# Optimization experiments

Hardware: AMD Instinct MI355X
Metric: run time of the kernel (lower is better)

Reference implementation:

```python
import jax, jax.numpy as jnp
import numpy as np

TAU = 1.0
EPS = 1e-06


def setup_inputs() -> dict:
    key = jax.random.key(0)
    batch = jax.random.normal(key, (8192, 256), dtype=jnp.float32)
    return {"batch": batch}


def reference(batch):
    n = batch.shape[0]
    half = n // 2
    # reorder: interleave first half and second half -> [x0, y0, x1, y1, ...]
    idx = jnp.stack([jnp.arange(half), jnp.arange(half) + half], axis=1).reshape(-1)
    x = batch[idx]                                   # [n, d]

    sim = x @ x.T                                    # [n, n] raw dot products
    norm = jnp.linalg.norm(x, axis=1, keepdims=True) # [n, 1]
    normmat = norm @ norm.T                          # [n, n]

    # denominator: zero the diagonal BEFORE exp (diag contributes exp(0)=1, as in torch code)
    mask = 1.0 - jnp.eye(n, dtype=x.dtype)
    den = jnp.sum(jnp.exp(mask * sim / (normmat + EPS) / TAU), axis=1)  # [n]

    # numerator: for row k, positive pair is (i, i+1) with i = 2*(k//2); no eps (faithful)
    i = (jnp.arange(n) // 2) * 2
    num = sim[i, i + 1] / normmat[i, i + 1]          # [n]

    loss = jnp.sum(-jnp.log(jnp.exp(num / TAU) / den)) / n
    return loss
```

## Files before the change

kernel.cpp:

```cpp
#include <hip/hip_runtime.h>
#include <hip/hip_bf16.h>


#define N_ROWS 8192
#define HALF   4096
#define DDIM   256
#define NBLK   64

typedef unsigned int   u32;
typedef unsigned short u16;
typedef __attribute__((ext_vector_type(4))) float f32x4;
typedef __attribute__((ext_vector_type(8))) short bf16x8;

__device__ __forceinline__ u16 f2bf(float f) {
    u32 u = __builtin_bit_cast(u32, f);
    u32 r = u + 0x7FFFu + ((u >> 16) & 1u);
    return (u16)(r >> 16);
}

__global__ __launch_bounds__(256) void prep_kernel(const float* __restrict__ x,
                                                   u16* __restrict__ xn,
                                                   float* __restrict__ norms,
                                                   float* __restrict__ dots) {
    const int w = threadIdx.x >> 6, l = threadIdx.x & 63;
    if (blockIdx.x < 2048) {
        const int row = blockIdx.x * 4 + w;
        const float4 v = reinterpret_cast<const float4*>(x + (size_t)row * DDIM)[l];
        float sq = v.x * v.x + v.y * v.y + v.z * v.z + v.w * v.w;
#pragma unroll
        for (int off = 1; off < 64; off <<= 1) sq += __shfl_xor(sq, off);
        const float norm = sqrtf(sq);
        if (l == 0) norms[row] = norm;
        const float rn = 1.0f / norm;
        ushort4 o;
        o.x = f2bf(v.x * rn); o.y = f2bf(v.y * rn);
        o.z = f2bf(v.z * rn); o.w = f2bf(v.w * rn);
        reinterpret_cast<ushort4*>(xn + (size_t)row * DDIM)[l] = o;
    } else {
        const int m = (blockIdx.x - 2048) * 4 + w;
        const float4 a = reinterpret_cast<const float4*>(x + (size_t)m * DDIM)[l];
        const float4 b = reinterpret_cast<const float4*>(x + (size_t)(m + HALF) * DDIM)[l];
        float s = a.x * b.x + a.y * b.y + a.z * b.z + a.w * b.w;
#pragma unroll
        for (int off = 1; off < 64; off <<= 1) s += __shfl_xor(s, off);
        if (l == 0) dots[m] = s;
    }
}

__global__ __launch_bounds__(256) void gram_kernel(const u16* __restrict__ xn,
                                                   float* __restrict__ part) {
    const int t = blockIdx.x;
    int bi = (int)(0.5f * (129.0f - sqrtf(16641.0f - 8.0f * (float)t)));
    if (bi > 0 && bi * (129 - bi) / 2 > t) --bi;
    if ((bi + 1) * (129 - (bi + 1)) / 2 <= t) ++bi;
    const int bj = bi + (t - bi * (129 - bi) / 2);
    const bool diagblk = (bi == bj);
    const int r0 = bi * 128, c0 = bj * 128;

    __shared__ __align__(16) char smem[32768];
    u16* As = (u16*)smem;
    u16* Bs = (u16*)(smem + 16384);

    const int tid = threadIdx.x;
    const int w = tid >> 6, l = tid & 63;
    const int wr = w >> 1, wc = w & 1;

    const f32x4 vzero = {0.f, 0.f, 0.f, 0.f};
    f32x4 acc[4][4];
#pragma unroll
    for (int m = 0; m < 4; ++m)
#pragma unroll
        for (int n = 0; n < 4; ++n) acc[m][n] = vzero;

    const int krow = l >> 3;
    const int kcol = (((l & 7) ^ krow) * 8);

    const int rsw = (l & 7) << 3;

    for (int ks = 0; ks < 4; ++ks) {
#pragma unroll
        for (int i = 0; i < 4; ++i) {
            const int rr = w * 32 + i * 8;
            const u16* ga = xn + (size_t)(r0 + rr + krow) * DDIM + ks * 64 + kcol;
            __builtin_amdgcn_global_load_lds(
                (const __attribute__((address_space(1))) u32*)ga,
                (__attribute__((address_space(3))) u32*)(As + rr * 64), 16, 0, 0);
            const u16* gb = xn + (size_t)(c0 + rr + krow) * DDIM + ks * 64 + kcol;
            __builtin_amdgcn_global_load_lds(
                (const __attribute__((address_space(1))) u32*)gb,
                (__attribute__((address_space(3))) u32*)(Bs + rr * 64), 16, 0, 0);
        }
        __syncthreads();
#pragma unroll
        for (int s = 0; s < 2; ++s) {
            bf16x8 a[4], b[4];
            const int koff = (s * 32 + (l >> 4) * 8) ^ rsw;
#pragma unroll
            for (int n = 0; n < 4; ++n)
                a[n] = *reinterpret_cast<const bf16x8*>(As + (wr * 64 + n * 16 + (l & 15)) * 64 + koff);
#pragma unroll
            for (int m = 0; m < 4; ++m)
                b[m] = *reinterpret_cast<const bf16x8*>(Bs + (wc * 64 + m * 16 + (l & 15)) * 64 + koff);
#pragma unroll
            for (int m = 0; m < 4; ++m)
#pragma unroll
                for (int n = 0; n < 4; ++n)
                    acc[m][n] = __builtin_amdgcn_mfma_f32_16x16x32_bf16(b[m], a[n], acc[m][n], 0, 0, 0);
        }
        __syncthreads();
    }

#pragma unroll
    for (int m = 0; m < 4; ++m)
#pragma unroll
        for (int n = 0; n < 4; ++n)
#pragma unroll
            for (int rg = 0; rg < 4; ++rg) {
                const float e = __expf(acc[m][n][rg]);
                if (diagblk) {
                    const int j_loc = wc * 64 + m * 16 + (l >> 4) * 4 + rg;
                    const int r_loc = wr * 64 + n * 16 + (l & 15);
                    acc[m][n][rg] = (j_loc == r_loc) ? 1.0f : e;
                } else {
                    acc[m][n][rg] = e;
                }
            }

    float* cs  = (float*)smem;
    float* dsh = (float*)(smem + 24576);

#pragma unroll
    for (int n = 0; n < 4; ++n) {
        float s = 0.f;
#pragma unroll
        for (int m = 0; m < 4; ++m)
#pragma unroll
            for (int rg = 0; rg < 4; ++rg) s += acc[m][n][rg];
        s += __shfl_xor(s, 16);
        s += __shfl_xor(s, 32);
        if (l < 16) dsh[wc * 128 + wr * 64 + n * 16 + l] = s;
    }

    if (!diagblk) {
#pragma unroll
        for (int m = 0; m < 4; ++m)
#pragma unroll
            for (int rg = 0; rg < 4; ++rg) {
                const float s = acc[m][0][rg] + acc[m][1][rg] + acc[m][2][rg] + acc[m][3][rg];
                const int j_loc = wc * 64 + m * 16 + (l >> 4) * 4 + rg;
                cs[(wr * 128 + j_loc) * 17 + (l & 15)] = s;
            }
    }
    __syncthreads();

    if (tid < 128) {
        const float den = dsh[tid] + dsh[128 + tid];
        part[(size_t)bj * N_ROWS + r0 + tid] = den;
        if (!diagblk) {
            float c = 0.f;
#pragma unroll
            for (int k = 0; k < 16; ++k)
                c += cs[tid * 17 + k] + cs[(128 + tid) * 17 + k];
            part[(size_t)bi * N_ROWS + c0 + tid] = c;
        }
    }
}

__global__ __launch_bounds__(256) void fin1_kernel(const float* __restrict__ part,
                                                   const float* __restrict__ norms,
                                                   const float* __restrict__ dots,
                                                   float* __restrict__ bsum) {
    const int b = blockIdx.x, t = threadIdx.x;
    const int r = b * 256 + t;
    float den = 0.f;
#pragma unroll 8
    for (int bj = 0; bj < 64; ++bj) den += part[(size_t)bj * N_ROWS + r];
    float local = logf(den);
    if (t < 128) {
        const int m = b * 128 + t;
        local -= 2.0f * dots[m] / (norms[m] * norms[m + HALF]);
    }
#pragma unroll
    for (int off = 1; off < 64; off <<= 1) local += __shfl_xor(local, off);
    __shared__ float wsum[4];
    if ((t & 63) == 0) wsum[t >> 6] = local;
    __syncthreads();
    if (t == 0) bsum[b] = wsum[0] + wsum[1] + wsum[2] + wsum[3];
}

__global__ void fin2_kernel(const float* __restrict__ bsum, float* __restrict__ out) {
    const int t = threadIdx.x;
    float v = (t < 32) ? bsum[t] : 0.f;
#pragma unroll
    for (int off = 1; off < 32; off <<= 1) v += __shfl_xor(v, off);
    if (t == 0) out[0] = v / (float)N_ROWS;
}

extern "C" void kernel_launch(void* const* d_in, const int* in_sizes, int n_in,
                              void* d_out, int out_size, void* d_ws, size_t ws_size,
                              hipStream_t stream) {
    const float* x = (const float*)d_in[0];
    float* out = (float*)d_out;
    char* ws = (char*)d_ws;

    u16*   xn    = (u16*)ws;
    float* norms = (float*)(ws + 4194304);
    float* dots  = (float*)(ws + 4227072);
    float* part  = (float*)(ws + 4243456);
    float* bsum  = (float*)(ws + 6340608);

    prep_kernel<<<3072, 256, 0, stream>>>(x, xn, norms, dots);
    gram_kernel<<<(NBLK * (NBLK + 1)) / 2, 256, 0, stream>>>(xn, part);
    fin1_kernel<<<32, 256, 0, stream>>>(part, norms, dots, bsum);
    fin2_kernel<<<1, 64, 0, stream>>>(bsum, out);
}
```

Baseline: 41.68 us.

## Quantize normalized rows to FP8 e4m3 and use scaled f8f6f4 MFMA for Gram

The normalized rows are now stored as FP8 e4m3, prescaled by 16, instead of bf16. The Gram matrix is computed with the 16x16x128 scaled f8f6f4 MFMA, and the result is rescaled by 1/256 before exp. This halves global and LDS traffic and the number of K steps, and each MFMA covers four times more K. The cost is much lower precision in the cosine similarities, which feed exp and the loss sum and may push the loss outside tolerance.

New measurement: 34.11 us. -18.2%, faster.

```diff
diff --git a/kernel.cpp b/kernel.cpp
--- a/kernel.cpp
+++ b/kernel.cpp
@@ -8,18 +8,28 @@
 #define NBLK   64
 
 typedef unsigned int   u32;
-typedef unsigned short u16;
+typedef unsigned char  u8;
 typedef __attribute__((ext_vector_type(4))) float f32x4;
-typedef __attribute__((ext_vector_type(8))) short bf16x8;
-
-__device__ __forceinline__ u16 f2bf(float f) {
-    u32 u = __builtin_bit_cast(u32, f);
-    u32 r = u + 0x7FFFu + ((u >> 16) & 1u);
-    return (u16)(r >> 16);
+typedef __attribute__((ext_vector_type(4))) int   i32x4;
+typedef __attribute__((ext_vector_type(8))) int   i32x8;
+
+__device__ __forceinline__ u32 f2e4m3(float f) {
+    const u32 u = __builtin_bit_cast(u32, f);
+    const u32 s = (u >> 24) & 0x80u;
+    const float af = fabsf(f);
+    if (af < 0.015625f) {
+        const int mi = (int)rintf(af * 512.0f);
+        return s | (u32)mi;
+    }
+    u32 keep = (u & 0x7FFFFFFFu) >> 20;
+    const u32 rem = u & 0xFFFFFu;
+    keep += (rem > 0x80000u) || (rem == 0x80000u && (keep & 1u));
+    const int ef = (int)(keep >> 3) - 120;
+    return s | ((u32)ef << 3) | (keep & 7u);
 }
 
 __global__ __launch_bounds__(256) void prep_kernel(const float* __restrict__ x,
-                                                   u16* __restrict__ xn,
+                                                   u8* __restrict__ xq,
                                                    float* __restrict__ norms,
                                                    float* __restrict__ dots) {
     const int w = threadIdx.x >> 6, l = threadIdx.x & 63;
@@ -31,11 +41,10 @@
         for (int off = 1; off < 64; off <<= 1) sq += __shfl_xor(sq, off);
         const float norm = sqrtf(sq);
         if (l == 0) norms[row] = norm;
-        const float rn = 1.0f / norm;
-        ushort4 o;
-        o.x = f2bf(v.x * rn); o.y = f2bf(v.y * rn);
-        o.z = f2bf(v.z * rn); o.w = f2bf(v.w * rn);
-        reinterpret_cast<ushort4*>(xn + (size_t)row * DDIM)[l] = o;
+        const float rs = 16.0f / norm;
+        const u32 pk = f2e4m3(v.x * rs) | (f2e4m3(v.y * rs) << 8) |
+                       (f2e4m3(v.z * rs) << 16) | (f2e4m3(v.w * rs) << 24);
+        reinterpret_cast<u32*>(xq + (size_t)row * DDIM)[l] = pk;
     } else {
         const int m = (blockIdx.x - 2048) * 4 + w;
         const float4 a = reinterpret_cast<const float4*>(x + (size_t)m * DDIM)[l];
@@ -47,7 +56,7 @@
     }
 }
 
-__global__ __launch_bounds__(256) void gram_kernel(const u16* __restrict__ xn,
+__global__ __launch_bounds__(256) void gram_kernel(const u8* __restrict__ xq,
                                                    float* __restrict__ part) {
     const int t = blockIdx.x;
     int bi = (int)(0.5f * (129.0f - sqrtf(16641.0f - 8.0f * (float)t)));
@@ -58,8 +67,8 @@
     const int r0 = bi * 128, c0 = bj * 128;
 
     __shared__ __align__(16) char smem[32768];
-    u16* As = (u16*)smem;
-    u16* Bs = (u16*)(smem + 16384);
+    u8* As = (u8*)smem;
+    u8* Bs = (u8*)(smem + 16384);
 
     const int tid = threadIdx.x;
     const int w = tid >> 6, l = tid & 63;
@@ -73,39 +82,46 @@
         for (int n = 0; n < 4; ++n) acc[m][n] = vzero;
 
     const int krow = l >> 3;
-    const int kcol = (((l & 7) ^ krow) * 8);
-
-    const int rsw = (l & 7) << 3;
-
-    for (int ks = 0; ks < 4; ++ks) {
+    const int kbyte = ((l & 7) ^ krow) * 16;
+    const int r7 = l & 7;
+    const int kq2 = (l >> 4) * 2;
+
+    for (int ks = 0; ks < 2; ++ks) {
 #pragma unroll
         for (int i = 0; i < 4; ++i) {
             const int rr = w * 32 + i * 8;
-            const u16* ga = xn + (size_t)(r0 + rr + krow) * DDIM + ks * 64 + kcol;
+            const u8* ga = xq + (size_t)(r0 + rr + krow) * DDIM + ks * 128 + kbyte;
             __builtin_amdgcn_global_load_lds(
                 (const __attribute__((address_space(1))) u32*)ga,
-                (__attribute__((address_space(3))) u32*)(As + rr * 64), 16, 0, 0);
-            const u16* gb = xn + (size_t)(c0 + rr + krow) * DDIM + ks * 64 + kcol;
+                (__attribute__((address_space(3))) u32*)(As + rr * 128), 16, 0, 0);
+            const u8* gb = xq + (size_t)(c0 + rr + krow) * DDIM + ks * 128 + kbyte;
             __builtin_amdgcn_global_load_lds(
                 (const __attribute__((address_space(1))) u32*)gb,
-                (__attribute__((address_space(3))) u32*)(Bs + rr * 64), 16, 0, 0);
+                (__attribute__((address_space(3))) u32*)(Bs + rr * 128), 16, 0, 0);
         }
         __syncthreads();
-#pragma unroll
-        for (int s = 0; s < 2; ++s) {
-            bf16x8 a[4], b[4];
-            const int koff = (s * 32 + (l >> 4) * 8) ^ rsw;
-#pragma unroll
-            for (int n = 0; n < 4; ++n)
-                a[n] = *reinterpret_cast<const bf16x8*>(As + (wr * 64 + n * 16 + (l & 15)) * 64 + koff);
+
+        i32x8 bfr[4];
+#pragma unroll
+        for (int m = 0; m < 4; ++m) {
+            const u8* rowp = Bs + (wc * 64 + m * 16 + (l & 15)) * 128;
+            const i32x4 lo = *reinterpret_cast<const i32x4*>(rowp + ((kq2 ^ r7) << 4));
+            const i32x4 hi = *reinterpret_cast<const i32x4*>(rowp + (((kq2 + 1) ^ r7) << 4));
+            bfr[m][0] = lo[0]; bfr[m][1] = lo[1]; bfr[m][2] = lo[2]; bfr[m][3] = lo[3];
+            bfr[m][4] = hi[0]; bfr[m][5] = hi[1]; bfr[m][6] = hi[2]; bfr[m][7] = hi[3];
+        }
+#pragma unroll
+        for (int n = 0; n < 4; ++n) {
+            const u8* rowp = As + (wr * 64 + n * 16 + (l & 15)) * 128;
+            const i32x4 lo = *reinterpret_cast<const i32x4*>(rowp + ((kq2 ^ r7) << 4));
+            const i32x4 hi = *reinterpret_cast<const i32x4*>(rowp + (((kq2 + 1) ^ r7) << 4));
+            i32x8 afr;
+            afr[0] = lo[0]; afr[1] = lo[1]; afr[2] = lo[2]; afr[3] = lo[3];
+            afr[4] = hi[0]; afr[5] = hi[1]; afr[6] = hi[2]; afr[7] = hi[3];
 #pragma unroll
             for (int m = 0; m < 4; ++m)
-                b[m] = *reinterpret_cast<const bf16x8*>(Bs + (wc * 64 + m * 16 + (l & 15)) * 64 + koff);
-#pragma unroll
-            for (int m = 0; m < 4; ++m)
-#pragma unroll
-                for (int n = 0; n < 4; ++n)
-                    acc[m][n] = __builtin_amdgcn_mfma_f32_16x16x32_bf16(b[m], a[n], acc[m][n], 0, 0, 0);
+                acc[m][n] = __builtin_amdgcn_mfma_scale_f32_16x16x128_f8f6f4(
+                    bfr[m], afr, acc[m][n], 0, 0, 0, 0x7F7F7F7F, 0, 0x7F7F7F7F);
         }
         __syncthreads();
     }
@@ -116,7 +132,7 @@
         for (int n = 0; n < 4; ++n)
 #pragma unroll
             for (int rg = 0; rg < 4; ++rg) {
-                const float e = __expf(acc[m][n][rg]);
+                const float e = __expf(acc[m][n][rg] * 0.00390625f);
                 if (diagblk) {
                     const int j_loc = wc * 64 + m * 16 + (l >> 4) * 4 + rg;
                     const int r_loc = wr * 64 + n * 16 + (l & 15);
@@ -203,14 +219,14 @@
     float* out = (float*)d_out;
     char* ws = (char*)d_ws;
 
-    u16*   xn    = (u16*)ws;
-    float* norms = (float*)(ws + 4194304);
-    float* dots  = (float*)(ws + 4227072);
-    float* part  = (float*)(ws + 4243456);
-    float* bsum  = (float*)(ws + 6340608);
-
-    prep_kernel<<<3072, 256, 0, stream>>>(x, xn, norms, dots);
-    gram_kernel<<<(NBLK * (NBLK + 1)) / 2, 256, 0, stream>>>(xn, part);
+    u8*    xq    = (u8*)ws;
+    float* norms = (float*)(ws + 2097152);
+    float* dots  = (float*)(ws + 2129920);
+    float* part  = (float*)(ws + 2146304);
+    float* bsum  = (float*)(ws + 4243456);
+
+    prep_kernel<<<3072, 256, 0, stream>>>(x, xq, norms, dots);
+    gram_kernel<<<(NBLK * (NBLK + 1)) / 2, 256, 0, stream>>>(xq, part);
     fin1_kernel<<<32, 256, 0, stream>>>(part, norms, dots, bsum);
     fin2_kernel<<<1, 64, 0, stream>>>(bsum, out);
 }
```
